# Kernel optimization log

Measured on AMD Instinct MI355X. Metric: run time of the kernel, lower is better.

The kernel has to match this reference:

```python
import jax, jax.numpy as jnp
import numpy as np

B, I, O, NB, H = 32768, 256, 256, 256, 16  # batch, input_dim, output_dim, num_basis, hidden

def setup_inputs() -> dict:
    key = jax.random.key(0)
    ks = jax.random.split(key, 6)
    x = jax.random.normal(ks[0], (B, I), dtype=jnp.float32)
    weights = jax.random.normal(ks[1], (O, I, NB), dtype=jnp.float32)
    # Stacked per-input-dim basis MLPs: Linear(1,16) -> SiLU -> Linear(16,1)
    # Kaiming-uniform-ish init scale; exact init irrelevant for correctness baseline
    w1 = jax.random.normal(ks[2], (I, H), dtype=jnp.float32)          # Linear(1,16).weight squeezed
    b1 = jax.random.normal(ks[3], (I, H), dtype=jnp.float32) * 0.1
    w2 = jax.random.normal(ks[4], (I, H), dtype=jnp.float32) / np.sqrt(H)  # Linear(16,1).weight squeezed
    b2 = jax.random.normal(ks[5], (I,), dtype=jnp.float32) * 0.1
    return {"x": x, "weights": weights, "w1": w1, "b1": b1, "w2": w2, "b2": b2}

def reference(x, weights, w1, b1, w2, b2):
    # phi_i(x[:, i]) for all i at once. hidden: [B, I, H]
    hidden = jax.nn.silu(x[:, :, None] * w1[None, :, :] + b1[None, :, :])
    phi = jnp.einsum('bih,ih->bi', hidden, w2) + b2[None, :]  # [B, I]
    # weight * basis_output summed over last dim == sum_k weights[o,i,k] * phi
    wsum = jnp.sum(weights, axis=-1)  # [O, I]
    return jnp.einsum('bi,oi->bo', phi, wsum)  # [B, O]
```

## Files before the change

### kernel.cpp

```cpp
#include <hip/hip_runtime.h>


#define B_DIM 32768
#define I_DIM 256
#define O_DIM 256
#define NB_DIM 256

typedef __bf16 bf16x8 __attribute__((ext_vector_type(8)));
typedef float f32x4 __attribute__((ext_vector_type(4)));

__device__ __forceinline__ size_t wpack_idx(int o, int ii) {
    const int l = (o & 15) | (((ii >> 3) & 3) << 4);
    return (size_t)((((o >> 4) * 8 + (ii >> 5)) * 64) + l) * 8 + (ii & 7);
}

__global__ __launch_bounds__(256) void k_wsum(
    const float* __restrict__ wt,
    __bf16* __restrict__ wpack)
{
    const int wave = (int)(threadIdx.x >> 6);
    const int lane = (int)(threadIdx.x & 63u);
    const int pbase = ((int)blockIdx.x * 4 + wave) * 4;
    #pragma unroll
    for (int j = 0; j < 4; ++j) {
        const int p = pbase + j;
        const float4 v = ((const float4*)(wt + (size_t)p * NB_DIM))[lane];
        float s = (v.x + v.y) + (v.z + v.w);
        #pragma unroll
        for (int off = 32; off; off >>= 1) s += __shfl_down(s, off, 64);
        if (lane == 0) wpack[wpack_idx(p >> 8, p & 255)] = (__bf16)s;
    }
}

__global__ __launch_bounds__(512, 4) void k_fused(
    const float* __restrict__ x,
    const float* __restrict__ w1,
    const float* __restrict__ b1,
    const float* __restrict__ w2,
    const float* __restrict__ b2,
    const __bf16* __restrict__ wpack,
    float* __restrict__ out)
{
    __shared__ uint4 atile4[2048];
    char* atile = (char*)atile4;
    const int tid = (int)threadIdx.x;

    {
        const int i = tid & 255;
        const int half = tid >> 8;
        const float4* w1v = (const float4*)(w1 + i * 16);
        const float4* b1v = (const float4*)(b1 + i * 16);
        const float4* w2v = (const float4*)(w2 + i * 16);
        const float4 w1a = w1v[0], w1b = w1v[1], w1c = w1v[2], w1d = w1v[3];
        const float4 b1a = b1v[0], b1b = b1v[1], b1c = b1v[2], b1d = b1v[3];
        const float4 w2a = w2v[0], w2b = w2v[1], w2c = w2v[2], w2d = w2v[3];
        const float b2r = b2[i];
        const size_t xbase = (size_t)((int)blockIdx.x * 64 + half * 32) * I_DIM + i;

        for (int rr = 0; rr < 32; rr += 2) {
            const float xv0 = x[xbase + (size_t)rr * I_DIM];
            const float xv1 = x[xbase + (size_t)(rr + 1) * I_DIM];
            float acc0 = b2r, acc1 = b2r;
#define KAN_STEP(WV, BV, DV)                                                   \
            {                                                                  \
                float z0 = fmaf(xv0, WV, BV), z1 = fmaf(xv1, WV, BV);          \
                float s0 = __builtin_amdgcn_rcpf(                              \
                    1.0f + __builtin_amdgcn_exp2f(z0 * -1.44269504f));         \
                float s1 = __builtin_amdgcn_rcpf(                              \
                    1.0f + __builtin_amdgcn_exp2f(z1 * -1.44269504f));         \
                acc0 = fmaf(z0 * s0, DV, acc0);                                \
                acc1 = fmaf(z1 * s1, DV, acc1);                                \
            }
            KAN_STEP(w1a.x, b1a.x, w2a.x) KAN_STEP(w1a.y, b1a.y, w2a.y)
            KAN_STEP(w1a.z, b1a.z, w2a.z) KAN_STEP(w1a.w, b1a.w, w2a.w)
            KAN_STEP(w1b.x, b1b.x, w2b.x) KAN_STEP(w1b.y, b1b.y, w2b.y)
            KAN_STEP(w1b.z, b1b.z, w2b.z) KAN_STEP(w1b.w, b1b.w, w2b.w)
            KAN_STEP(w1c.x, b1c.x, w2c.x) KAN_STEP(w1c.y, b1c.y, w2c.y)
            KAN_STEP(w1c.z, b1c.z, w2c.z) KAN_STEP(w1c.w, b1c.w, w2c.w)
            KAN_STEP(w1d.x, b1d.x, w2d.x) KAN_STEP(w1d.y, b1d.y, w2d.y)
            KAN_STEP(w1d.z, b1d.z, w2d.z) KAN_STEP(w1d.w, b1d.w, w2d.w)
#undef KAN_STEP
            const int rl0 = half * 32 + rr, rl1 = rl0 + 1;
            const int a0 = (rl0 * 512 + i * 2) ^ ((rl0 & 7) << 4);
            const int a1 = (rl1 * 512 + i * 2) ^ ((rl1 & 7) << 4);
            *(__bf16*)(atile + a0) = (__bf16)acc0;
            *(__bf16*)(atile + a1) = (__bf16)acc1;
        }
    }
    __syncthreads();

    const int lane = tid & 63, wave = tid >> 6;
    const int wm = wave >> 2, wn = wave & 3;
    const int rowsel = lane & 15;
    const int kgrp = lane >> 4;

    f32x4 acc[2][4] = {};
    #pragma unroll
    for (int kx = 0; kx < 8; ++kx) {
        bf16x8 a[2], bb[4];
        #pragma unroll
        for (int t = 0; t < 2; ++t) {
            const int r = wm * 32 + t * 16 + rowsel;
            const int boff = (r << 9) + ((kx * 64 + kgrp * 16) ^ ((r & 7) << 4));
            a[t] = *(const bf16x8*)(atile + boff);
        }
        #pragma unroll
        for (int t = 0; t < 4; ++t) {
            const int nf = wn * 4 + t;
            bb[t] = *(const bf16x8*)(wpack + (size_t)(((nf * 8 + kx) * 64) + lane) * 8);
        }
        #pragma unroll
        for (int mi = 0; mi < 2; ++mi)
            #pragma unroll
            for (int ni = 0; ni < 4; ++ni)
                acc[mi][ni] = __builtin_amdgcn_mfma_f32_16x16x32_bf16(
                    a[mi], bb[ni], acc[mi][ni], 0, 0, 0);
    }

    const int m_base = (int)blockIdx.x * 64 + wm * 32;
    const int n_base = wn * 64;
    const int r0 = (lane >> 4) * 4, c = lane & 15;
    #pragma unroll
    for (int mi = 0; mi < 2; ++mi)
        #pragma unroll
        for (int ni = 0; ni < 4; ++ni)
            #pragma unroll
            for (int rr = 0; rr < 4; ++rr)
                out[(size_t)(m_base + mi * 16 + r0 + rr) * O_DIM + n_base + ni * 16 + c] =
                    acc[mi][ni][rr];
}

extern "C" void kernel_launch(void* const* d_in, const int* in_sizes, int n_in,
                              void* d_out, int out_size, void* d_ws, size_t ws_size,
                              hipStream_t stream) {
    const float* x  = (const float*)d_in[0];
    const float* wt = (const float*)d_in[1];
    const float* w1 = (const float*)d_in[2];
    const float* b1 = (const float*)d_in[3];
    const float* w2 = (const float*)d_in[4];
    const float* b2 = (const float*)d_in[5];
    float* out = (float*)d_out;

    __bf16* wpack = (__bf16*)d_ws;

    hipLaunchKernelGGL(k_wsum, dim3(4096), dim3(256), 0, stream, wt, wpack);
    hipLaunchKernelGGL(k_fused, dim3(512), dim3(512), 0, stream,
                       x, w1, b1, w2, b2, wpack, out);
}
```

Baseline: 170.9 us.

## Halve fused tile rows, raise occupancy, batch wsum reductions per wave

The fused kernel now handles 32 batch rows per block instead of 64, with half the shared A tile. Each wave owns a 32x32 output slice, and the launch bound is raised to 8 blocks per CU with twice as many blocks. The wsum kernel now has each wave load and reduce 8 rows together, interleaving the shuffle chains to hide latency. The smaller tiles cut per-block work and LDS use to improve occupancy, at the cost of reloading B fragments from global twice as often across blocks and more repeated per-thread parameter loads.

```diff
diff --git a/kernel.cpp b/kernel.cpp
--- a/kernel.cpp
+++ b/kernel.cpp
@@ -20,19 +20,28 @@
 {
     const int wave = (int)(threadIdx.x >> 6);
     const int lane = (int)(threadIdx.x & 63u);
-    const int pbase = ((int)blockIdx.x * 4 + wave) * 4;
+    const int p0 = ((int)blockIdx.x * 4 + wave) * 8;
+    float s[8];
     #pragma unroll
-    for (int j = 0; j < 4; ++j) {
-        const int p = pbase + j;
-        const float4 v = ((const float4*)(wt + (size_t)p * NB_DIM))[lane];
-        float s = (v.x + v.y) + (v.z + v.w);
+    for (int j = 0; j < 8; ++j) {
+        const float4 v = ((const float4*)(wt + (size_t)(p0 + j) * NB_DIM))[lane];
+        s[j] = (v.x + v.y) + (v.z + v.w);
+    }
+    #pragma unroll
+    for (int off = 32; off; off >>= 1) {
         #pragma unroll
-        for (int off = 32; off; off >>= 1) s += __shfl_down(s, off, 64);
-        if (lane == 0) wpack[wpack_idx(p >> 8, p & 255)] = (__bf16)s;
+        for (int j = 0; j < 8; ++j) s[j] += __shfl_down(s[j], off, 64);
+    }
+    if (lane == 0) {
+        #pragma unroll
+        for (int j = 0; j < 8; ++j) {
+            const int p = p0 + j;
+            wpack[wpack_idx(p >> 8, p & 255)] = (__bf16)s[j];
+        }
     }
 }
 
-__global__ __launch_bounds__(512, 4) void k_fused(
+__global__ __launch_bounds__(512, 8) void k_fused(
     const float* __restrict__ x,
     const float* __restrict__ w1,
     const float* __restrict__ b1,
@@ -41,7 +50,7 @@
     const __bf16* __restrict__ wpack,
     float* __restrict__ out)
 {
-    __shared__ uint4 atile4[2048];
+    __shared__ uint4 atile4[1024];
     char* atile = (char*)atile4;
     const int tid = (int)threadIdx.x;
 
@@ -55,9 +64,9 @@
         const float4 b1a = b1v[0], b1b = b1v[1], b1c = b1v[2], b1d = b1v[3];
         const float4 w2a = w2v[0], w2b = w2v[1], w2c = w2v[2], w2d = w2v[3];
         const float b2r = b2[i];
-        const size_t xbase = (size_t)((int)blockIdx.x * 64 + half * 32) * I_DIM + i;
+        const size_t xbase = (size_t)((int)blockIdx.x * 32 + half * 16) * I_DIM + i;
 
-        for (int rr = 0; rr < 32; rr += 2) {
+        for (int rr = 0; rr < 16; rr += 2) {
             const float xv0 = x[xbase + (size_t)rr * I_DIM];
             const float xv1 = x[xbase + (size_t)(rr + 1) * I_DIM];
             float acc0 = b2r, acc1 = b2r;
@@ -80,7 +89,7 @@
             KAN_STEP(w1d.x, b1d.x, w2d.x) KAN_STEP(w1d.y, b1d.y, w2d.y)
             KAN_STEP(w1d.z, b1d.z, w2d.z) KAN_STEP(w1d.w, b1d.w, w2d.w)
 #undef KAN_STEP
-            const int rl0 = half * 32 + rr, rl1 = rl0 + 1;
+            const int rl0 = half * 16 + rr, rl1 = rl0 + 1;
             const int a0 = (rl0 * 512 + i * 2) ^ ((rl0 & 7) << 4);
             const int a1 = (rl1 * 512 + i * 2) ^ ((rl1 & 7) << 4);
             *(__bf16*)(atile + a0) = (__bf16)acc0;
@@ -90,40 +99,39 @@
     __syncthreads();
 
     const int lane = tid & 63, wave = tid >> 6;
-    const int wm = wave >> 2, wn = wave & 3;
     const int rowsel = lane & 15;
     const int kgrp = lane >> 4;
 
-    f32x4 acc[2][4] = {};
+    f32x4 acc[2][2] = {};
     #pragma unroll
     for (int kx = 0; kx < 8; ++kx) {
-        bf16x8 a[2], bb[4];
+        bf16x8 a[2], bb[2];
         #pragma unroll
         for (int t = 0; t < 2; ++t) {
-            const int r = wm * 32 + t * 16 + rowsel;
-            const int boff = (r << 9) + ((kx * 64 + kgrp * 16) ^ ((r & 7) << 4));
+            const int r = t * 16 + rowsel;
+            const int boff = r * 512 + ((kx * 64 + kgrp * 16) ^ ((r & 7) << 4));
             a[t] = *(const bf16x8*)(atile + boff);
         }
         #pragma unroll
-        for (int t = 0; t < 4; ++t) {
-            const int nf = wn * 4 + t;
+        for (int t = 0; t < 2; ++t) {
+            const int nf = wave * 2 + t;
             bb[t] = *(const bf16x8*)(wpack + (size_t)(((nf * 8 + kx) * 64) + lane) * 8);
         }
         #pragma unroll
         for (int mi = 0; mi < 2; ++mi)
             #pragma unroll
-            for (int ni = 0; ni < 4; ++ni)
+            for (int ni = 0; ni < 2; ++ni)
                 acc[mi][ni] = __builtin_amdgcn_mfma_f32_16x16x32_bf16(
                     a[mi], bb[ni], acc[mi][ni], 0, 0, 0);
     }
 
-    const int m_base = (int)blockIdx.x * 64 + wm * 32;
-    const int n_base = wn * 64;
+    const int m_base = (int)blockIdx.x * 32;
+    const int n_base = wave * 32;
     const int r0 = (lane >> 4) * 4, c = lane & 15;
     #pragma unroll
     for (int mi = 0; mi < 2; ++mi)
         #pragma unroll
-        for (int ni = 0; ni < 4; ++ni)
+        for (int ni = 0; ni < 2; ++ni)
             #pragma unroll
             for (int rr = 0; rr < 4; ++rr)
                 out[(size_t)(m_base + mi * 16 + r0 + rr) * O_DIM + n_base + ni * 16 + c] =
@@ -143,7 +151,7 @@
 
     __bf16* wpack = (__bf16*)d_ws;
 
-    hipLaunchKernelGGL(k_wsum, dim3(4096), dim3(256), 0, stream, wt, wpack);
-    hipLaunchKernelGGL(k_fused, dim3(512), dim3(512), 0, stream,
+    hipLaunchKernelGGL(k_wsum, dim3(2048), dim3(256), 0, stream, wt, wpack);
+    hipLaunchKernelGGL(k_fused, dim3(1024), dim3(512), 0, stream,
                        x, w1, b1, w2, b2, wpack, out);
 }
```

Measured after the change: 166.6 us. -2.5%, faster.
